# Performance work log

Measured on AMD Instinct MI355X. Metric: run time of the kernel, lower is better.

The kernel has to match this reference:

```python
import jax, jax.numpy as jnp
import numpy as np

# Config constants (match init_kwargs / config)
B = 16        # config.BATCH_SIZE
T = 2048      # config.TRAIN_LEN
C = 256       # input channels (input_shape[-1])
K = 8         # kernel_size
F = 256       # nb_filters
DIL = 4       # dilation_rate


def setup_inputs() -> dict:
    key = jax.random.key(0)
    k1, k2, k3 = jax.random.split(key, 3)
    inputs = jax.random.normal(k1, (B, T, C), dtype=jnp.float32)
    kernel = jax.random.normal(k2, (C, K, F), dtype=jnp.float32) * 0.05
    bias = jax.random.normal(k3, (F,), dtype=jnp.float32) * 0.05
    return {"inputs": inputs, "kernel": kernel, "bias": bias}


def reference(inputs, kernel, bias):
    # Original TF layer computes, per (b,t,k,f):
    #   raw[b,t,k,f] = sum_c (x[b,t,c] * kernel[c,k,f] + bias[f])
    #               = conv[b,t,k,f] + C * bias[f]
    # (bias is added BEFORE the reduce_sum over the channel axis, so it is
    #  scaled by C — we reproduce that quirk faithfully.)
    # Then each (t,k) slice is scatter-added to output time t + k*dilation
    # (the gather_nd + zero-pad construction in TF implements exactly this
    #  dilated transposed-conv scatter; non-matching positions gather zeros),
    # and finally the last T timesteps are kept.
    Bq, Tq, Cq = inputs.shape
    Kq, Fq = kernel.shape[1], kernel.shape[2]
    conv = jnp.einsum('btc,ckf->btkf', inputs, kernel) + jnp.asarray(Cq, inputs.dtype) * bias
    L = Tq + (Kq - 1) * DIL  # final_time_len
    # scatter positions: out[i + j*DIL] += conv[:, i, j, :]
    pos = (jnp.arange(Tq)[:, None] + DIL * jnp.arange(Kq)[None, :]).reshape(-1)  # (T*K,)
    out = jnp.zeros((Bq, L, Fq), dtype=conv.dtype)
    out = out.at[:, pos, :].add(conv.reshape(Bq, Tq * Kq, Fq))
    return out[:, -Tq:, :]
```

## Files before the change

kernel.cpp:

```cpp
#include <hip/hip_runtime.h>
#include <hip/hip_bf16.h>


#define B_    16
#define T_    2048
#define C_    256
#define KT    8
#define F_    256
#define DILL  4
#define SH    28
#define BT    128
#define ROWS  (BT + SH)

typedef __attribute__((ext_vector_type(8))) short short8;
typedef __attribute__((ext_vector_type(4))) float floatx4;

__global__ __launch_bounds__(256) void wprep_kernel(const float* __restrict__ W,
                                                    ushort* __restrict__ Wf) {
    const int tid  = threadIdx.x;
    const int fid  = blockIdx.x * 4 + (tid >> 6);
    const int lane = tid & 63;
    const int g    = fid & 15;
    const int cs   = (fid >> 4) & 7;
    const int j    = fid >> 7;
    const int c0   = cs * 32 + (lane >> 4) * 8;
    const int f    = g * 16 + (lane & 15);
    short8 pk;
    #pragma unroll
    for (int i = 0; i < 8; ++i) {
        __hip_bfloat16 h = __float2bfloat16(W[((c0 + i) * KT + j) * F_ + f]);
        pk[i] = *reinterpret_cast<const short*>(&h);
    }
    *reinterpret_cast<short8*>(Wf + fid * 512 + lane * 8) = pk;
}

__global__ __launch_bounds__(512, 2) void deconv_kernel(
        const float* __restrict__ x, const ushort* __restrict__ Wf,
        const float* __restrict__ bias, float* __restrict__ out) {
    __shared__ ushort xs[ROWS * C_];
    const int t0  = blockIdx.x * BT;
    const int b   = blockIdx.y;
    const int tid = threadIdx.x;

    for (int idx = tid; idx < ROWS * 32; idx += 512) {
        const int row = idx >> 5, cb = idx & 31;
        const int t = t0 + row;
        float v[8] = {0.f,0.f,0.f,0.f,0.f,0.f,0.f,0.f};
        if (t < T_) {
            const float4* p = reinterpret_cast<const float4*>(
                x + ((b * T_ + t) * C_ + cb * 8));
            float4 u0 = p[0], u1 = p[1];
            v[0]=u0.x; v[1]=u0.y; v[2]=u0.z; v[3]=u0.w;
            v[4]=u1.x; v[5]=u1.y; v[6]=u1.z; v[7]=u1.w;
        }
        short8 pk;
        #pragma unroll
        for (int i = 0; i < 8; ++i) {
            __hip_bfloat16 h = __float2bfloat16(v[i]);
            pk[i] = *reinterpret_cast<const short*>(&h);
        }
        const int sc = cb ^ (row & 7);
        *reinterpret_cast<short8*>(&xs[row * C_ + sc * 8]) = pk;
    }

    const int lane = tid & 63, wave = tid >> 6;
    const int l16 = lane & 15, q = lane >> 4;

    float bf2[2];
    #pragma unroll
    for (int nf = 0; nf < 2; ++nf) bf2[nf] = bias[wave * 32 + nf * 16 + l16];

    __syncthreads();

    floatx4 acc[8][2];
    #pragma unroll
    for (int mf = 0; mf < 8; ++mf)
        #pragma unroll
        for (int nf = 0; nf < 2; ++nf)
            acc[mf][nf] = (floatx4){0.f, 0.f, 0.f, 0.f};

    const ushort* wbase = Wf + wave * 1024 + lane * 8;

#define LOAD_A(s_, arr) do {                                              \
        const int j_ = (s_) >> 3, cs_ = (s_) & 7;                         \
        const int shift_ = SH - 4 * j_;                                   \
        _Pragma("unroll")                                                 \
        for (int mf = 0; mf < 8; ++mf) {                                  \
            const int row_ = mf * 16 + l16 + shift_;                      \
            const int ch_  = ((cs_ << 2) + q) ^ (row_ & 7);               \
            arr[mf] = *reinterpret_cast<const short8*>(                   \
                &xs[row_ * C_ + ch_ * 8]);                                \
        } } while (0)

#define LOAD_B(s_, arr) do {                                              \
        const ushort* p_ = wbase + (s_) * 8192;                           \
        _Pragma("unroll")                                                 \
        for (int nf = 0; nf < 2; ++nf)                                    \
            arr[nf] = *reinterpret_cast<const short8*>(p_ + nf * 512);    \
        } while (0)

#define DO_MFMA(aa, bb) do {                                              \
        _Pragma("unroll")                                                 \
        for (int mf = 0; mf < 8; ++mf)                                    \
            _Pragma("unroll")                                             \
            for (int nf = 0; nf < 2; ++nf)                                \
                acc[mf][nf] = __builtin_amdgcn_mfma_f32_16x16x32_bf16(    \
                    aa[mf], bb[nf], acc[mf][nf], 0, 0, 0);                \
        } while (0)

    short8 a0[8], b0[2], a1[8], b1[2];
    LOAD_A(0, a0); LOAD_B(0, b0);
    LOAD_A(1, a1); LOAD_B(1, b1);

    for (int s = 0; s < 64; s += 2) {
        DO_MFMA(a0, b0);
        const int sp2 = (s + 2) & 63;
        LOAD_A(sp2, a0); LOAD_B(sp2, b0);
        DO_MFMA(a1, b1);
        const int sp3 = (s + 3) & 63;
        LOAD_A(sp3, a1); LOAD_B(sp3, b1);
    }

    #pragma unroll
    for (int nf = 0; nf < 2; ++nf) {
        const int f = wave * 32 + nf * 16 + l16;
        #pragma unroll
        for (int mf = 0; mf < 8; ++mf) {
            #pragma unroll
            for (int r = 0; r < 4; ++r) {
                const int t = t0 + mf * 16 + q * 4 + r;
                const int jmin = (t < T_ - SH) ? 0 : (((t - (T_ - SH)) >> 2) + 1);
                out[(b * T_ + t) * F_ + f] =
                    acc[mf][nf][r] + (float)(8 - jmin) * 256.0f * bf2[nf];
            }
        }
    }
#undef LOAD_A
#undef LOAD_B
#undef DO_MFMA
}

extern "C" void kernel_launch(void* const* d_in, const int* in_sizes, int n_in,
                              void* d_out, int out_size, void* d_ws, size_t ws_size,
                              hipStream_t stream) {
    const float* x    = (const float*)d_in[0];
    const float* W    = (const float*)d_in[1];
    const float* bias = (const float*)d_in[2];
    float* out = (float*)d_out;
    ushort* Wf = (ushort*)d_ws;

    wprep_kernel<<<256, 256, 0, stream>>>(W, Wf);
    dim3 grid(T_ / BT, B_);
    deconv_kernel<<<grid, 512, 0, stream>>>(x, Wf, bias, out);
}
```

Measured before the change: 49.51 us.

## Double-buffer input channel chunks in LDS to overlap global loads with MFMA

The whole 156x256 bf16 input tile is no longer staged once up front. Input is now streamed in 32-channel chunks through a double-buffered LDS area with a padded row stride of 40, and the loop is reordered to channel-chunk outer, tap inner. The global loads for the next chunk are issued into registers before the MFMAs on the current chunk, so load latency overlaps compute. This also shrinks LDS per block, which may allow more resident blocks. The cost is one barrier per chunk, and the weight layout is permuted to match the new loop order.

```diff
diff --git a/kernel.cpp b/kernel.cpp
--- a/kernel.cpp
+++ b/kernel.cpp
@@ -7,10 +7,12 @@
 #define C_    256
 #define KT    8
 #define F_    256
-#define DILL  4
 #define SH    28
 #define BT    128
 #define ROWS  (BT + SH)
+#define CH    32
+#define LSTR  40
+#define CHUNK (ROWS * LSTR)
 
 typedef __attribute__((ext_vector_type(8))) short short8;
 typedef __attribute__((ext_vector_type(4))) float floatx4;
@@ -21,8 +23,8 @@
     const int fid  = blockIdx.x * 4 + (tid >> 6);
     const int lane = tid & 63;
     const int g    = fid & 15;
-    const int cs   = (fid >> 4) & 7;
-    const int j    = fid >> 7;
+    const int j    = (fid >> 4) & 7;
+    const int cs   = fid >> 7;
     const int c0   = cs * 32 + (lane >> 4) * 8;
     const int f    = g * 16 + (lane & 15);
     short8 pk;
@@ -34,91 +36,111 @@
     *reinterpret_cast<short8*>(Wf + fid * 512 + lane * 8) = pk;
 }
 
+__device__ inline short8 cvt8(float4 a, float4 b) {
+    float v[8] = {a.x, a.y, a.z, a.w, b.x, b.y, b.z, b.w};
+    short8 r;
+    #pragma unroll
+    for (int i = 0; i < 8; ++i) {
+        __hip_bfloat16 h = __float2bfloat16(v[i]);
+        r[i] = *reinterpret_cast<const short*>(&h);
+    }
+    return r;
+}
+
 __global__ __launch_bounds__(512, 2) void deconv_kernel(
         const float* __restrict__ x, const ushort* __restrict__ Wf,
         const float* __restrict__ bias, float* __restrict__ out) {
-    __shared__ ushort xs[ROWS * C_];
-    const int t0  = blockIdx.x * BT;
-    const int b   = blockIdx.y;
-    const int tid = threadIdx.x;
+    __shared__ ushort xs[2 * CHUNK];
+    const int t0   = blockIdx.x * BT;
+    const int b    = blockIdx.y;
+    const int tid  = threadIdx.x;
+    const int lane = tid & 63, wave = tid >> 6;
+    const int l16  = lane & 15, q = lane >> 4;
 
-    for (int idx = tid; idx < ROWS * 32; idx += 512) {
-        const int row = idx >> 5, cb = idx & 31;
-        const int t = t0 + row;
-        float v[8] = {0.f,0.f,0.f,0.f,0.f,0.f,0.f,0.f};
-        if (t < T_) {
-            const float4* p = reinterpret_cast<const float4*>(
-                x + ((b * T_ + t) * C_ + cb * 8));
-            float4 u0 = p[0], u1 = p[1];
-            v[0]=u0.x; v[1]=u0.y; v[2]=u0.z; v[3]=u0.w;
-            v[4]=u1.x; v[5]=u1.y; v[6]=u1.z; v[7]=u1.w;
-        }
-        short8 pk;
-        #pragma unroll
-        for (int i = 0; i < 8; ++i) {
-            __hip_bfloat16 h = __float2bfloat16(v[i]);
-            pk[i] = *reinterpret_cast<const short*>(&h);
-        }
-        const int sc = cb ^ (row & 7);
-        *reinterpret_cast<short8*>(&xs[row * C_ + sc * 8]) = pk;
-    }
+    const int r0  = tid >> 2,  qd0 = tid & 3;
+    const int idx1 = tid + 512;
+    const int r1  = idx1 >> 2, qd1 = idx1 & 3;
 
-    const int lane = tid & 63, wave = tid >> 6;
-    const int l16 = lane & 15, q = lane >> 4;
+    float4 R[2][2];
+
+#define STAGE_LOAD(cs_) do {                                                   \
+        R[0][0] = make_float4(0,0,0,0); R[0][1] = make_float4(0,0,0,0);        \
+        R[1][0] = make_float4(0,0,0,0); R[1][1] = make_float4(0,0,0,0);        \
+        if (t0 + r0 < T_) {                                                    \
+            const float4* p = reinterpret_cast<const float4*>(                 \
+                x + ((size_t)(b * T_ + t0 + r0) * C_ + (cs_) * CH + qd0 * 8)); \
+            R[0][0] = p[0]; R[0][1] = p[1];                                    \
+        }                                                                      \
+        if (idx1 < ROWS * 4 && t0 + r1 < T_) {                                 \
+            const float4* p = reinterpret_cast<const float4*>(                 \
+                x + ((size_t)(b * T_ + t0 + r1) * C_ + (cs_) * CH + qd1 * 8)); \
+            R[1][0] = p[0]; R[1][1] = p[1];                                    \
+        } } while (0)
+
+#define STAGE_WRITE(buf_) do {                                                 \
+        ushort* d_ = xs + (buf_) * CHUNK;                                      \
+        *reinterpret_cast<short8*>(d_ + r0 * LSTR + qd0 * 8) =                 \
+            cvt8(R[0][0], R[0][1]);                                            \
+        if (idx1 < ROWS * 4)                                                   \
+            *reinterpret_cast<short8*>(d_ + r1 * LSTR + qd1 * 8) =             \
+                cvt8(R[1][0], R[1][1]);                                        \
+        } while (0)
 
     float bf2[2];
-    #pragma unroll
-    for (int nf = 0; nf < 2; ++nf) bf2[nf] = bias[wave * 32 + nf * 16 + l16];
-
-    __syncthreads();
+    bf2[0] = bias[wave * 32 + l16];
+    bf2[1] = bias[wave * 32 + 16 + l16];
 
     floatx4 acc[8][2];
     #pragma unroll
-    for (int mf = 0; mf < 8; ++mf)
-        #pragma unroll
-        for (int nf = 0; nf < 2; ++nf)
-            acc[mf][nf] = (floatx4){0.f, 0.f, 0.f, 0.f};
+    for (int mf = 0; mf < 8; ++mf) {
+        acc[mf][0] = (floatx4){0.f, 0.f, 0.f, 0.f};
+        acc[mf][1] = (floatx4){0.f, 0.f, 0.f, 0.f};
+    }
 
-    const ushort* wbase = Wf + wave * 1024 + lane * 8;
+    const ushort* wb = Wf + (wave * 2) * 512 + lane * 8;
 
-#define LOAD_A(s_, arr) do {                                              \
-        const int j_ = (s_) >> 3, cs_ = (s_) & 7;                         \
-        const int shift_ = SH - 4 * j_;                                   \
-        _Pragma("unroll")                                                 \
-        for (int mf = 0; mf < 8; ++mf) {                                  \
-            const int row_ = mf * 16 + l16 + shift_;                      \
-            const int ch_  = ((cs_ << 2) + q) ^ (row_ & 7);               \
-            arr[mf] = *reinterpret_cast<const short8*>(                   \
-                &xs[row_ * C_ + ch_ * 8]);                                \
+#define LOAD_A(buf_, j_, arr) do {                                             \
+        const ushort* s_ = xs + (buf_) * CHUNK                                 \
+                           + (l16 + (SH - 4 * (j_))) * LSTR + q * 8;           \
+        _Pragma("unroll")                                                      \
+        for (int mf = 0; mf < 8; ++mf)                                         \
+            arr[mf] = *reinterpret_cast<const short8*>(s_ + mf * 16 * LSTR);   \
+        } while (0)
+
+#define LOAD_B(cs_, j_, arr) do {                                              \
+        const ushort* p_ = wb + (size_t)(cs_) * 65536 + (j_) * 8192;           \
+        arr[0] = *reinterpret_cast<const short8*>(p_);                         \
+        arr[1] = *reinterpret_cast<const short8*>(p_ + 512);                   \
+        } while (0)
+
+#define DO_MFMA(aa, bb) do {                                                   \
+        _Pragma("unroll")                                                      \
+        for (int mf = 0; mf < 8; ++mf) {                                       \
+            acc[mf][0] = __builtin_amdgcn_mfma_f32_16x16x32_bf16(              \
+                aa[mf], bb[0], acc[mf][0], 0, 0, 0);                           \
+            acc[mf][1] = __builtin_amdgcn_mfma_f32_16x16x32_bf16(              \
+                aa[mf], bb[1], acc[mf][1], 0, 0, 0);                           \
         } } while (0)
 
-#define LOAD_B(s_, arr) do {                                              \
-        const ushort* p_ = wbase + (s_) * 8192;                           \
-        _Pragma("unroll")                                                 \
-        for (int nf = 0; nf < 2; ++nf)                                    \
-            arr[nf] = *reinterpret_cast<const short8*>(p_ + nf * 512);    \
-        } while (0)
+    STAGE_LOAD(0);
+    STAGE_WRITE(0);
+    __syncthreads();
 
-#define DO_MFMA(aa, bb) do {                                              \
-        _Pragma("unroll")                                                 \
-        for (int mf = 0; mf < 8; ++mf)                                    \
-            _Pragma("unroll")                                             \
-            for (int nf = 0; nf < 2; ++nf)                                \
-                acc[mf][nf] = __builtin_amdgcn_mfma_f32_16x16x32_bf16(    \
-                    aa[mf], bb[nf], acc[mf][nf], 0, 0, 0);                \
-        } while (0)
+    for (int cs = 0; cs < 8; ++cs) {
+        const int buf = cs & 1;
+        if (cs < 7) STAGE_LOAD(cs + 1);
 
-    short8 a0[8], b0[2], a1[8], b1[2];
-    LOAD_A(0, a0); LOAD_B(0, b0);
-    LOAD_A(1, a1); LOAD_B(1, b1);
+        short8 a[2][8], bb[2][2];
+        LOAD_A(buf, 0, a[0]); LOAD_B(cs, 0, bb[0]);
+        LOAD_A(buf, 1, a[1]); LOAD_B(cs, 1, bb[1]);
+        #pragma unroll
+        for (int j = 0; j < 8; ++j) {
+            DO_MFMA(a[j & 1], bb[j & 1]);
+            if (j < 6) { LOAD_A(buf, j + 2, a[j & 1]); LOAD_B(cs, j + 2, bb[j & 1]); }
+        }
 
-    for (int s = 0; s < 64; s += 2) {
-        DO_MFMA(a0, b0);
-        const int sp2 = (s + 2) & 63;
-        LOAD_A(sp2, a0); LOAD_B(sp2, b0);
-        DO_MFMA(a1, b1);
-        const int sp3 = (s + 3) & 63;
-        LOAD_A(sp3, a1); LOAD_B(sp3, b1);
+        if (cs < 7) STAGE_WRITE(buf ^ 1);
+        __syncthreads();
     }
 
     #pragma unroll
@@ -135,6 +157,8 @@
             }
         }
     }
+#undef STAGE_LOAD
+#undef STAGE_WRITE
 #undef LOAD_A
 #undef LOAD_B
 #undef DO_MFMA
```

Measured after the change: 53.01 us. 1.07x slower.
